# Kernel optimization log

Hardware: AMD Instinct MI355X
Metric: run time of the kernel (lower is better)

The kernel has to match this reference:

```python
import jax, jax.numpy as jnp
import numpy as np
import math

B, S, HID = 4, 2048, 1024
H, D = 16, HID // 16


def setup_inputs() -> dict:
    key = jax.random.key(0)
    ks = jax.random.split(key, 6)
    scale = 0.02
    inp = {
        "hidden_states": jax.random.normal(ks[0], (B, S, HID), dtype=jnp.float32),
        "Wq": jax.random.normal(ks[1], (HID, HID), dtype=jnp.float32) * scale,
        "bq": jnp.zeros((HID,), dtype=jnp.float32),
        "Wk1": jax.random.normal(ks[2], (HID, HID), dtype=jnp.float32) * scale,
        "bk1": jnp.zeros((HID,), dtype=jnp.float32),
        "Wk2": jax.random.normal(ks[3], (HID, HID), dtype=jnp.float32) * scale,
        "bk2": jnp.zeros((HID,), dtype=jnp.float32),
        "Wv1": jax.random.normal(ks[4], (HID, HID), dtype=jnp.float32) * scale,
        "bv1": jnp.zeros((HID,), dtype=jnp.float32),
        "Wv2": jax.random.normal(ks[5], (HID, HID), dtype=jnp.float32) * scale,
        "bv2": jnp.zeros((HID,), dtype=jnp.float32),
    }
    return inp


def _heads(x):
    # [B, S, HID] -> [B, H, S, D]
    return x.reshape(B, S, H, D).transpose(0, 2, 1, 3)


def reference(hidden_states, Wq, bq, Wk1, bk1, Wk2, bk2, Wv1, bv1, Wv2, bv2):
    # nn.Linear uses y = x @ W^T + b
    q = _heads(hidden_states @ Wq.T + bq)
    k1 = _heads(hidden_states @ Wk1.T + bk1)
    k2 = _heads(hidden_states @ Wk2.T + bk2)
    v1 = _heads(hidden_states @ Wv1.T + bv1)
    v2 = _heads(hidden_states @ Wv2.T + bv2)

    inv_sqrt_d = 1.0 / math.sqrt(D)
    scores = jnp.einsum('bhqd,bhkd->bhqk', q, k1) * inv_sqrt_d  # [B,H,S,S]
    probs = jax.nn.softmax(scores, axis=-1)
    ctx = jnp.einsum('bhqk,bhkd->bhqd', probs, v1)              # [B,H,S,D]
    ctx = jnp.einsum('bhqd,bhkd->bhqk', ctx, k2)                # [B,H,S,S]
    ctx = jnp.einsum('bhqk,bhkd->bhqd', ctx, v2)                # [B,H,S,D]
    # [B,H,S,D] -> [B,S,HID]
    return ctx.transpose(0, 2, 1, 3).reshape(B, S, HID)
```

## Files before the change

kernel.cpp:

```cpp
#include <hip/hip_runtime.h>
#include <hip/hip_bf16.h>

#define HIDD 1024
#define BATCH 4
#define SEQ 2048
#define NHEAD 16
#define HD 64
#define NW 5
#define MROWS (BATCH*SEQ)
#define NCOLS (NW*HIDD)

typedef __attribute__((ext_vector_type(8))) short bf16x8;
typedef __attribute__((ext_vector_type(4))) float f32x4;
typedef __attribute__((ext_vector_type(16))) float f32x16;
typedef __attribute__((ext_vector_type(4))) unsigned int uint4v;

__device__ __forceinline__ unsigned short f2b(float f) {
    __hip_bfloat16 h = __float2bfloat16(f);
    return __builtin_bit_cast(unsigned short, h);
}
__device__ __forceinline__ float b2f(unsigned short u) {
    __hip_bfloat16 h = __builtin_bit_cast(__hip_bfloat16, u);
    return __bfloat162float(h);
}

#if __has_builtin(__builtin_amdgcn_exp2f)
#define EXP2(x) __builtin_amdgcn_exp2f(x)
#else
#define EXP2(x) exp2f(x)
#endif

typedef __attribute__((address_space(1))) const void gvoid;
typedef __attribute__((address_space(3))) void lvoid;
__device__ __forceinline__ void gload16(const void* src, void* dst) {
    __builtin_amdgcn_global_load_lds((gvoid*)src, (lvoid*)dst, 16, 0, 0);
}

__global__ void cvt_kernel(const float* __restrict__ X,
                           const float* __restrict__ W0, const float* __restrict__ W1,
                           const float* __restrict__ W2, const float* __restrict__ W3,
                           const float* __restrict__ W4,
                           unsigned short* __restrict__ Xb, unsigned short* __restrict__ Wb)
{
    const int XN = MROWS * HIDD / 4;
    const int WN = HIDD * HIDD / 4;
    int i = blockIdx.x * 256 + threadIdx.x;
    if (i >= XN + 5 * WN) return;
    const float* src; unsigned short* dst; int off;
    if (i < XN) { src = X; dst = Xb; off = i; }
    else {
        int j = i - XN; int w = j / WN; int r = j - w * WN;
        src = (w == 0 ? W0 : w == 1 ? W1 : w == 2 ? W2 : w == 3 ? W3 : W4);
        dst = Wb + (long)w * HIDD * HIDD; off = r;
    }
    float4 v = ((const float4*)src)[off];
    short4 o;
    o.x = (short)f2b(v.x); o.y = (short)f2b(v.y);
    o.z = (short)f2b(v.z); o.w = (short)f2b(v.w);
    ((short4*)dst)[off] = o;
}

#define READ_A(buf, kh, mh) \
    _Pragma("unroll") \
    for (int mt = 0; mt < 4; ++mt) \
        af[mt] = *(const bf16x8*)((const char*)As[buf][kh] + \
                  (wr * 128 + (mh) * 64 + mt * 16 + q) * 64 + ((g ^ csw) << 4));
#define READ_B(buf, kh) \
    _Pragma("unroll") \
    for (int nt = 0; nt < 4; ++nt) \
        bfr[nt] = *(const bf16x8*)((const char*)Bs[buf][kh] + \
                  (wc * 64 + nt * 16 + q) * 64 + ((g ^ csw) << 4));
#define MFMA_Q(mh) \
    __builtin_amdgcn_s_setprio(1); \
    _Pragma("unroll") \
    for (int mt = 0; mt < 4; ++mt) \
    _Pragma("unroll") \
    for (int nt = 0; nt < 4; ++nt) \
        acc[(mh) * 4 + mt][nt] = __builtin_amdgcn_mfma_f32_16x16x32_bf16( \
            af[mt], bfr[nt], acc[(mh) * 4 + mt][nt], 0, 0, 0); \
    __builtin_amdgcn_s_setprio(0);

__global__ __launch_bounds__(512, 2) void gemm_proj(
    const unsigned short* __restrict__ Xb, const unsigned short* __restrict__ Wb,
    const float* __restrict__ pb0, const float* __restrict__ pb1, const float* __restrict__ pb2,
    const float* __restrict__ pb3, const float* __restrict__ pb4,
    unsigned short* __restrict__ C)
{
    __shared__ __align__(16) unsigned short As[2][2][256 * 32];
    __shared__ __align__(16) unsigned short Bs[2][2][256 * 32];
    int tid = threadIdx.x;
    int n = blockIdx.x;
    int xcd = n & 7, op = n >> 3;
    int ntile = (op < 16) ? 2 : 1;
    int lane = tid & 63, w = tid >> 6;
    int wr = w >> 2, wc = w & 3;
    int q = lane & 15, g = lane >> 4;
    int csw = (q >> 1) & 3;
    int srow = tid >> 2;
    int scol = ((tid & 3) ^ ((tid >> 3) & 3)) * 8;

    for (int tix = 0; tix < ntile; ++tix) {
        int o = op + tix * 64;
        int bm = xcd * 4 + (o & 3);
        int bn = o >> 2;

        if (tix) {
            asm volatile("s_waitcnt lgkmcnt(0)" ::: "memory");
            asm volatile("s_barrier" ::: "memory");
        }

        f32x4 acc[8][4] = {};
        const unsigned short* Ag = Xb + (long)(bm * 256) * HIDD;
        const unsigned short* Bg = Wb + (long)(bn * 256) * HIDD;

        auto stage = [&](const unsigned short* G, unsigned short* slot, int kc) {
#pragma unroll
            for (int l = 0; l < 2; ++l)
                gload16(G + (long)(l * 128 + srow) * HIDD + kc + scol,
                        (char*)slot + (l * 512 + tid) * 16);
        };

        stage(Ag, As[0][0], 0);
        stage(Bg, Bs[0][0], 0);
        stage(Ag, As[0][1], 32);
        stage(Bg, Bs[0][1], 32);
        stage(Ag, As[1][0], 64);
        stage(Bg, Bs[1][0], 64);

        for (int t = 0; t < 16; ++t) {
            int buf = t & 1;
            int kc1 = ((t + 1) & 15) * 64;
            int kc2 = ((t + 2) & 15) * 64;
            bf16x8 af[4], bfr[4];
            asm volatile("s_waitcnt vmcnt(8)" ::: "memory");
            asm volatile("s_waitcnt lgkmcnt(0)" ::: "memory");
            asm volatile("s_barrier" ::: "memory");
            READ_A(buf, 0, 0)
            READ_B(buf, 0)
            stage(Ag, As[buf ^ 1][1], kc1 + 32);
            MFMA_Q(0)
            READ_A(buf, 0, 1)
            stage(Bg, Bs[buf ^ 1][1], kc1 + 32);
            MFMA_Q(1)
            asm volatile("s_waitcnt vmcnt(8)" ::: "memory");
            asm volatile("s_waitcnt lgkmcnt(0)" ::: "memory");
            asm volatile("s_barrier" ::: "memory");
            READ_A(buf, 1, 0)
            READ_B(buf, 1)
            stage(Ag, As[buf][0], kc2);
            MFMA_Q(0)
            READ_A(buf, 1, 1)
            stage(Bg, Bs[buf][0], kc2);
            MFMA_Q(1)
        }

        int ncol0 = bn * 256 + wc * 64 + q;
        const float* bp = (bn < 4 ? pb0 : bn < 8 ? pb1 : bn < 12 ? pb2 : bn < 16 ? pb3 : pb4);
#pragma unroll
        for (int nt = 0; nt < 4; ++nt) {
            int ncol = ncol0 + nt * 16;
            float bv = bp[ncol & 1023];
#pragma unroll
            for (int mt = 0; mt < 8; ++mt) {
                int row = bm * 256 + wr * 128 + mt * 16 + g * 4;
#pragma unroll
                for (int r = 0; r < 4; ++r)
                    C[(long)(row + r) * NCOLS + ncol] = f2b(acc[mt][nt][r] + bv);
            }
        }
    }
}

#define QSCALE 0.180336880f
#define LDV 72
#define NT (SEQ / 64)

__global__ __launch_bounds__(512, 2) void flash1(
    const unsigned short* __restrict__ C, unsigned short* __restrict__ ctx)
{
    __shared__ unsigned short Ks[2][64 * 64];
    __shared__ unsigned short Vs[2][64 * LDV];
    __shared__ float Lbuf[8][32];
    int tid = threadIdx.x;
    int lane = tid & 63, w = tid >> 6;
    int q32 = lane & 31, hi = lane >> 5;
    int n = blockIdx.x;
    int qt = (n >> 3) & 7;
    int bh = (n & 7) * 8 + (n >> 6);
    int b = bh >> 4, h = bh & 15;
    long rowbase = (long)(b * SEQ) * NCOLS;
    int s0 = qt * 256;

    const unsigned short* Kg = C + rowbase + 1 * HIDD + h * 64;
    const unsigned short* Vg = C + rowbase + 3 * HIDD + h * 64;

    int krlo = lane >> 3;
    int kch  = (lane & 7) ^ krlo;
    int kp = tid & 31, dc = tid >> 5;
    int rsw = q32 & 7;

    bf16x8 qreg[4];
    {
        const unsigned short* Qp = C + rowbase + (long)(s0 + w * 32 + q32) * NCOLS + h * 64;
#pragma unroll
        for (int s = 0; s < 4; ++s) {
            bf16x8 v = *(const bf16x8*)(Qp + s * 16 + hi * 8);
#pragma unroll
            for (int j = 0; j < 8; j++)
                v[j] = (short)f2b(b2f((unsigned short)v[j]) * QSCALE);
            qreg[s] = v;
        }
    }

    gload16(Kg + (long)(w * 8 + krlo) * NCOLS + kch * 8,
            (char*)Ks[0] + w * 1024 + (lane << 4));
    if (tid < 256) {
        const unsigned short* vsrc = Vg + (long)(2 * kp) * NCOLS + dc * 8;
        bf16x8 v0 = *(const bf16x8*)vsrc;
        bf16x8 v1 = *(const bf16x8*)(vsrc + NCOLS);
        unsigned int* VsW = (unsigned int*)Vs[0];
#pragma unroll
        for (int j = 0; j < 8; j++) {
            unsigned int pk = ((unsigned int)(unsigned short)v0[j]) |
                              (((unsigned int)(unsigned short)v1[j]) << 16);
            VsW[(dc * 8 + j) * (LDV / 2) + kp] = pk;
        }
    }
    __syncthreads();

    f32x16 O0 = {}, O1 = {};
    float l_run = 0.f;

    auto body = [&](int kt, int cur, int nxt) {
        int ktn = (kt + 1) & (NT - 1);
        gload16(Kg + (long)(ktn * 64 + w * 8 + krlo) * NCOLS + kch * 8,
                (char*)Ks[nxt] + w * 1024 + (lane << 4));
        bf16x8 nv0 = {}, nv1 = {};
        if (tid < 256) {
            const unsigned short* nsrc = Vg + (long)(ktn * 64 + 2 * kp) * NCOLS + dc * 8;
            nv0 = *(const bf16x8*)nsrc;
            nv1 = *(const bf16x8*)(nsrc + NCOLS);
        }

        float lsum = 0.f;
        __builtin_amdgcn_s_setprio(1);
#pragma unroll
        for (int kb = 0; kb < 2; ++kb) {
            f32x16 st = {};
#pragma unroll
            for (int s = 0; s < 4; ++s) {
                bf16x8 kf = *(const bf16x8*)((const char*)Ks[cur] +
                             ((kb * 32 + q32) << 7) + (((2 * s + hi) ^ rsw) << 4));
                st = __builtin_amdgcn_mfma_f32_32x32x16_bf16(kf, qreg[s], st, 0, 0, 0);
            }
            float e[16];
#pragma unroll
            for (int r = 0; r < 16; ++r) e[r] = EXP2(st[r]);
            lsum += (((e[0]+e[1])+(e[2]+e[3])) + ((e[4]+e[5])+(e[6]+e[7])))
                  + (((e[8]+e[9])+(e[10]+e[11])) + ((e[12]+e[13])+(e[14]+e[15])));
            unsigned int Cw[8];
#pragma unroll
            for (int p = 0; p < 8; ++p)
                asm("v_cvt_pk_bf16_f32 %0, %1, %2" : "=v"(Cw[p]) : "v"(e[2*p]), "v"(e[2*p+1]));
#pragma unroll
            for (int t2 = 0; t2 < 2; ++t2) {
                unsigned int a0 = Cw[t2*4+0], a1 = Cw[t2*4+1];
                unsigned int a2 = Cw[t2*4+2], a3 = Cw[t2*4+3];
                asm("v_permlane32_swap_b32 %0, %1" : "+v"(a0), "+v"(a2));
                asm("v_permlane32_swap_b32 %0, %1" : "+v"(a1), "+v"(a3));
                uint4v aw; aw[0] = a0; aw[1] = a1; aw[2] = a2; aw[3] = a3;
                bf16x8 af = __builtin_bit_cast(bf16x8, aw);
                int t = kb * 2 + t2;
#pragma unroll
                for (int nt = 0; nt < 2; ++nt) {
                    bf16x8 vf = *(const bf16x8*)((const char*)Vs[cur] +
                                 (nt * 32 + q32) * (LDV * 2) + t * 32 + hi * 16);
                    if (nt == 0) O0 = __builtin_amdgcn_mfma_f32_32x32x16_bf16(af, vf, O0, 0, 0, 0);
                    else         O1 = __builtin_amdgcn_mfma_f32_32x32x16_bf16(af, vf, O1, 0, 0, 0);
                }
            }
        }
        __builtin_amdgcn_s_setprio(0);
        l_run += lsum;
        if (tid < 256) {
            unsigned int* VsWn = (unsigned int*)Vs[nxt];
#pragma unroll
            for (int j = 0; j < 8; ++j) {
                unsigned int pk = ((unsigned int)(unsigned short)nv0[j]) |
                                  (((unsigned int)(unsigned short)nv1[j]) << 16);
                VsWn[(dc * 8 + j) * (LDV / 2) + kp] = pk;
            }
        }
        __syncthreads();
    };

    for (int kt = 0; kt < NT; kt += 2) {
        body(kt, 0, 1);
        body(kt + 1, 1, 0);
    }

    l_run += __shfl_xor(l_run, 32);
    float linv = 1.f / l_run;
    Lbuf[w][q32] = linv;
    asm volatile("s_waitcnt lgkmcnt(0)" ::: "memory");
#pragma unroll
    for (int reg = 0; reg < 16; ++reg) {
        int row = (reg & 3) + 8 * (reg >> 2) + 4 * hi;
        float lr = Lbuf[w][row];
        unsigned short* dst = ctx + ((long)bh * SEQ + s0 + w * 32 + row) * 64 + q32;
        dst[0]  = f2b(O0[reg] * lr);
        dst[32] = f2b(O1[reg] * lr);
    }
}

#define LDT2 72
__global__ __launch_bounds__(256) void m_partial(
    const unsigned short* __restrict__ C, float* __restrict__ part)
{
    __shared__ unsigned short Kt[64 * LDT2];
    __shared__ unsigned short Vt[64 * LDT2];
    int tid = threadIdx.x;
    int lane = tid & 63, w = tid >> 6;
    int q32 = lane & 31, hi = lane >> 5;
    int sc = blockIdx.x;
    int bh = blockIdx.y; int b = bh >> 4, h = bh & 15;
    const unsigned short* K2 = C + (long)(b * SEQ) * NCOLS + 2 * HIDD + h * 64;
    const unsigned short* V2 = C + (long)(b * SEQ) * NCOLS + 4 * HIDD + h * 64;
    int kp = tid & 31, dc = tid >> 5;
    int d2h = w >> 1, d1h = w & 1;
    unsigned int* KtW = (unsigned int*)Kt;
    unsigned int* VtW = (unsigned int*)Vt;
    f32x16 acc = {};

    for (int tk = 0; tk < 4; ++tk) {
        int sbase = sc * 256 + tk * 64;
        if (tk) __syncthreads();
        const unsigned short* ks = K2 + (long)(sbase + 2 * kp) * NCOLS + dc * 8;
        bf16x8 k0 = *(const bf16x8*)ks, k1 = *(const bf16x8*)(ks + NCOLS);
        const unsigned short* vs = V2 + (long)(sbase + 2 * kp) * NCOLS + dc * 8;
        bf16x8 v0 = *(const bf16x8*)vs, v1 = *(const bf16x8*)(vs + NCOLS);
#pragma unroll
        for (int j = 0; j < 8; ++j) {
            KtW[(dc * 8 + j) * (LDT2 / 2) + kp] =
                (unsigned int)(unsigned short)k0[j] | ((unsigned int)(unsigned short)k1[j] << 16);
            VtW[(dc * 8 + j) * (LDT2 / 2) + kp] =
                (unsigned int)(unsigned short)v0[j] | ((unsigned int)(unsigned short)v1[j] << 16);
        }
        __syncthreads();
#pragma unroll
        for (int t = 0; t < 4; ++t) {
            bf16x8 afr = *(const bf16x8*)(Vt + (d2h * 32 + q32) * LDT2 + t * 16 + hi * 8);
            bf16x8 bfr = *(const bf16x8*)(Kt + (d1h * 32 + q32) * LDT2 + t * 16 + hi * 8);
            acc = __builtin_amdgcn_mfma_f32_32x32x16_bf16(afr, bfr, acc, 0, 0, 0);
        }
    }
    float* dst = part + ((long)(sc * 64 + bh) << 12);
#pragma unroll
    for (int reg = 0; reg < 16; ++reg) {
        int d2 = d2h * 32 + (reg & 3) + 8 * (reg >> 2) + 4 * hi;
        dst[d2 * 64 + d1h * 32 + q32] = acc[reg];
    }
}

__global__ void m_reduce(const float* __restrict__ part, float* __restrict__ MT)
{
    int i = blockIdx.x * 256 + threadIdx.x;
    if (i >= 64 * 4096) return;
    int bh = i >> 12, e = i & 4095;
    float s = 0.f;
#pragma unroll
    for (int sc = 0; sc < 8; sc++) s += part[((long)(sc * 64 + bh) << 12) + e];
    MT[i] = s;
}

#define LDF 72
#define LDM 68
__global__ __launch_bounds__(256) void final_out(
    const unsigned short* __restrict__ ctx, const float* __restrict__ MT,
    float* __restrict__ out)
{
    __shared__ unsigned short cs[64 * LDF];
    __shared__ float msT[64 * LDM];
    int tid = threadIdx.x;
    int st0 = blockIdx.x * 4;
    int bh = blockIdx.y; int b = bh >> 4, h = bh & 15;
    {
        const float* Msrc = MT + ((long)bh << 12);
        for (int i = tid; i < 4096; i += 256)
            msT[(i & 63) * LDM + (i >> 6)] = Msrc[i];
    }
    int s4 = (tid & 15) * 4, j4 = (tid >> 4) * 4;
    for (int ti = 0; ti < 4; ++ti) {
        int st = st0 + ti;
        if (ti) __syncthreads();
        {
            int i = tid >> 2, dcx = tid & 3;
            const unsigned short* src = ctx + ((long)bh * SEQ + st * 64 + i) * 64 + dcx * 16;
            *(int4*)(cs + i * LDF + dcx * 16)     = *(const int4*)src;
            *(int4*)(cs + i * LDF + dcx * 16 + 8) = *(const int4*)(src + 8);
        }
        __syncthreads();
        f32x4 acc[4] = {};
        for (int d1b = 0; d1b < 8; ++d1b) {
            bf16x8 cv[4];
#pragma unroll
            for (int r = 0; r < 4; ++r)
                cv[r] = *(const bf16x8*)(cs + (s4 + r) * LDF + d1b * 8);
#pragma unroll
            for (int dd = 0; dd < 8; ++dd) {
                f32x4 mj = *(const f32x4*)(msT + (d1b * 8 + dd) * LDM + j4);
#pragma unroll
                for (int r = 0; r < 4; ++r) {
                    float c = b2f((unsigned short)cv[r][dd]);
#pragma unroll
                    for (int j = 0; j < 4; ++j)
                        acc[r][j] += c * mj[j];
                }
            }
        }
        float* dst0 = out + (long)(b * SEQ + st * 64) * HIDD + h * 64;
#pragma unroll
        for (int r = 0; r < 4; ++r)
            *(f32x4*)(dst0 + (long)(s4 + r) * HIDD + j4) = acc[r];
    }
}

extern "C" void kernel_launch(void* const* d_in, const int* in_sizes, int n_in,
                              void* d_out, int out_size, void* d_ws, size_t ws_size,
                              hipStream_t stream)
{
    const float* X   = (const float*)d_in[0];
    const float* Wq  = (const float*)d_in[1];
    const float* bq  = (const float*)d_in[2];
    const float* Wk1 = (const float*)d_in[3];
    const float* bk1 = (const float*)d_in[4];
    const float* Wk2 = (const float*)d_in[5];
    const float* bk2 = (const float*)d_in[6];
    const float* Wv1 = (const float*)d_in[7];
    const float* bv1 = (const float*)d_in[8];
    const float* Wv2 = (const float*)d_in[9];
    const float* bv2 = (const float*)d_in[10];

    char* ws = (char*)d_ws;
    unsigned short* Xb  = (unsigned short*)(ws);
    unsigned short* Wb  = (unsigned short*)(ws + 16777216);
    unsigned short* C   = (unsigned short*)(ws + 27262976);
    unsigned short* ctx = (unsigned short*)(ws + 111149056);
    float* part         = (float*)(ws + 127926272);
    float* MT           = (float*)(ws + 136314880);
    float* out = (float*)d_out;

    cvt_kernel<<<dim3(13312), 256, 0, stream>>>(X, Wq, Wk1, Wk2, Wv1, Wv2, Xb, Wb);
    gemm_proj<<<dim3(512), 512, 0, stream>>>(Xb, Wb, bq, bk1, bk2, bv1, bv2, C);
    flash1<<<dim3(512), 512, 0, stream>>>(C, ctx);
    m_partial<<<dim3(8, 64), 256, 0, stream>>>(C, part);
    m_reduce<<<dim3(1024), 256, 0, stream>>>(part, MT);
    final_out<<<dim3(8, 64), 256, 0, stream>>>(ctx, MT, out);
}
```

Baseline: 243.6 us.

## Load projection GEMM B operand directly from global memory into registers

The weight (B) tile in the projection GEMM no longer goes through shared memory. Each wave now reads its B fragments straight from global memory into registers just before its MFMAs, and only the activation (A) tile is still staged in LDS, with the vmcnt waits adjusted to match. This removes the B staging traffic and halves the kernel's LDS use. In exchange, global-load latency is exposed directly in front of the MFMAs. Waves that share a column slice also fetch the same B data redundantly from cache instead of sharing one LDS copy.

```diff
diff --git a/kernel.cpp b/kernel.cpp
--- a/kernel.cpp
+++ b/kernel.cpp
@@ -65,11 +65,10 @@
     for (int mt = 0; mt < 4; ++mt) \
         af[mt] = *(const bf16x8*)((const char*)As[buf][kh] + \
                   (wr * 128 + (mh) * 64 + mt * 16 + q) * 64 + ((g ^ csw) << 4));
-#define READ_B(buf, kh) \
+#define READ_B_G(t, kh) \
     _Pragma("unroll") \
     for (int nt = 0; nt < 4; ++nt) \
-        bfr[nt] = *(const bf16x8*)((const char*)Bs[buf][kh] + \
-                  (wc * 64 + nt * 16 + q) * 64 + ((g ^ csw) << 4));
+        bfr[nt] = *(const bf16x8*)(Bw + (long)(nt * 16) * HIDD + (t) * 64 + (kh) * 32 + g * 8);
 #define MFMA_Q(mh) \
     __builtin_amdgcn_s_setprio(1); \
     _Pragma("unroll") \
@@ -87,7 +86,6 @@
     unsigned short* __restrict__ C)
 {
     __shared__ __align__(16) unsigned short As[2][2][256 * 32];
-    __shared__ __align__(16) unsigned short Bs[2][2][256 * 32];
     int tid = threadIdx.x;
     int n = blockIdx.x;
     int xcd = n & 7, op = n >> 3;
@@ -111,46 +109,41 @@
 
         f32x4 acc[8][4] = {};
         const unsigned short* Ag = Xb + (long)(bm * 256) * HIDD;
-        const unsigned short* Bg = Wb + (long)(bn * 256) * HIDD;
-
-        auto stage = [&](const unsigned short* G, unsigned short* slot, int kc) {
+        const unsigned short* Bw = Wb + (long)(bn * 256 + wc * 64 + q) * HIDD;
+
+        auto stage = [&](unsigned short* slot, int kc) {
 #pragma unroll
             for (int l = 0; l < 2; ++l)
-                gload16(G + (long)(l * 128 + srow) * HIDD + kc + scol,
+                gload16(Ag + (long)(l * 128 + srow) * HIDD + kc + scol,
                         (char*)slot + (l * 512 + tid) * 16);
         };
 
-        stage(Ag, As[0][0], 0);
-        stage(Bg, Bs[0][0], 0);
-        stage(Ag, As[0][1], 32);
-        stage(Bg, Bs[0][1], 32);
-        stage(Ag, As[1][0], 64);
-        stage(Bg, Bs[1][0], 64);
+        stage(As[0][0], 0);
+        stage(As[0][1], 32);
+        stage(As[1][0], 64);
 
         for (int t = 0; t < 16; ++t) {
             int buf = t & 1;
             int kc1 = ((t + 1) & 15) * 64;
             int kc2 = ((t + 2) & 15) * 64;
             bf16x8 af[4], bfr[4];
-            asm volatile("s_waitcnt vmcnt(8)" ::: "memory");
+            asm volatile("s_waitcnt vmcnt(2)" ::: "memory");
             asm volatile("s_waitcnt lgkmcnt(0)" ::: "memory");
             asm volatile("s_barrier" ::: "memory");
+            READ_B_G(t, 0)
             READ_A(buf, 0, 0)
-            READ_B(buf, 0)
-            stage(Ag, As[buf ^ 1][1], kc1 + 32);
+            stage(As[buf ^ 1][1], kc1 + 32);
             MFMA_Q(0)
             READ_A(buf, 0, 1)
-            stage(Bg, Bs[buf ^ 1][1], kc1 + 32);
             MFMA_Q(1)
-            asm volatile("s_waitcnt vmcnt(8)" ::: "memory");
+            asm volatile("s_waitcnt vmcnt(2)" ::: "memory");
             asm volatile("s_waitcnt lgkmcnt(0)" ::: "memory");
             asm volatile("s_barrier" ::: "memory");
+            READ_B_G(t, 1)
             READ_A(buf, 1, 0)
-            READ_B(buf, 1)
-            stage(Ag, As[buf][0], kc2);
+            stage(As[buf][0], kc2);
             MFMA_Q(0)
             READ_A(buf, 1, 1)
-            stage(Bg, Bs[buf][0], kc2);
             MFMA_Q(1)
         }
 
```

After: 293.6 us. 20.5% more time.

## Merge flash and K2V2 partial kernels into one launch, fold reduce into final

Applied to the files above, without the earlier changes.

Merges the flash attention kernel and the K2^T V2 partial-product kernel into a single launch of 1024 blocks, where the first 512 blocks run attention and the rest compute partials. The separate reduction kernel is removed, and final_out now sums the 8 partials itself while loading M. This cuts two kernel launches and lets the small partial work fill idle CUs during the flash tail. In exchange, the partial blocks run at 512 threads with half of them idle and share the flash kernel's larger LDS footprint, and every final_out block redundantly re-reduces its head's partials.

```diff
diff --git a/kernel.cpp b/kernel.cpp
--- a/kernel.cpp
+++ b/kernel.cpp
@@ -174,209 +174,203 @@
 #define QSCALE 0.180336880f
 #define LDV 72
 #define NT (SEQ / 64)
-
-__global__ __launch_bounds__(512, 2) void flash1(
-    const unsigned short* __restrict__ C, unsigned short* __restrict__ ctx)
+#define LDT2 72
+
+__global__ __launch_bounds__(512, 2) void flash_mp(
+    const unsigned short* __restrict__ C, unsigned short* __restrict__ ctx,
+    float* __restrict__ part)
 {
     __shared__ unsigned short Ks[2][64 * 64];
     __shared__ unsigned short Vs[2][64 * LDV];
     __shared__ float Lbuf[8][32];
-    int tid = threadIdx.x;
-    int lane = tid & 63, w = tid >> 6;
-    int q32 = lane & 31, hi = lane >> 5;
-    int n = blockIdx.x;
-    int qt = (n >> 3) & 7;
-    int bh = (n & 7) * 8 + (n >> 6);
-    int b = bh >> 4, h = bh & 15;
-    long rowbase = (long)(b * SEQ) * NCOLS;
-    int s0 = qt * 256;
-
-    const unsigned short* Kg = C + rowbase + 1 * HIDD + h * 64;
-    const unsigned short* Vg = C + rowbase + 3 * HIDD + h * 64;
-
-    int krlo = lane >> 3;
-    int kch  = (lane & 7) ^ krlo;
-    int kp = tid & 31, dc = tid >> 5;
-    int rsw = q32 & 7;
-
-    bf16x8 qreg[4];
-    {
-        const unsigned short* Qp = C + rowbase + (long)(s0 + w * 32 + q32) * NCOLS + h * 64;
-#pragma unroll
-        for (int s = 0; s < 4; ++s) {
-            bf16x8 v = *(const bf16x8*)(Qp + s * 16 + hi * 8);
-#pragma unroll
-            for (int j = 0; j < 8; j++)
-                v[j] = (short)f2b(b2f((unsigned short)v[j]) * QSCALE);
-            qreg[s] = v;
-        }
-    }
-
-    gload16(Kg + (long)(w * 8 + krlo) * NCOLS + kch * 8,
-            (char*)Ks[0] + w * 1024 + (lane << 4));
-    if (tid < 256) {
-        const unsigned short* vsrc = Vg + (long)(2 * kp) * NCOLS + dc * 8;
-        bf16x8 v0 = *(const bf16x8*)vsrc;
-        bf16x8 v1 = *(const bf16x8*)(vsrc + NCOLS);
-        unsigned int* VsW = (unsigned int*)Vs[0];
-#pragma unroll
-        for (int j = 0; j < 8; j++) {
-            unsigned int pk = ((unsigned int)(unsigned short)v0[j]) |
-                              (((unsigned int)(unsigned short)v1[j]) << 16);
-            VsW[(dc * 8 + j) * (LDV / 2) + kp] = pk;
-        }
-    }
-    __syncthreads();
-
-    f32x16 O0 = {}, O1 = {};
-    float l_run = 0.f;
-
-    auto body = [&](int kt, int cur, int nxt) {
-        int ktn = (kt + 1) & (NT - 1);
-        gload16(Kg + (long)(ktn * 64 + w * 8 + krlo) * NCOLS + kch * 8,
-                (char*)Ks[nxt] + w * 1024 + (lane << 4));
-        bf16x8 nv0 = {}, nv1 = {};
-        if (tid < 256) {
-            const unsigned short* nsrc = Vg + (long)(ktn * 64 + 2 * kp) * NCOLS + dc * 8;
-            nv0 = *(const bf16x8*)nsrc;
-            nv1 = *(const bf16x8*)(nsrc + NCOLS);
-        }
-
-        float lsum = 0.f;
-        __builtin_amdgcn_s_setprio(1);
-#pragma unroll
-        for (int kb = 0; kb < 2; ++kb) {
-            f32x16 st = {};
-#pragma unroll
-            for (int s = 0; s < 4; ++s) {
-                bf16x8 kf = *(const bf16x8*)((const char*)Ks[cur] +
-                             ((kb * 32 + q32) << 7) + (((2 * s + hi) ^ rsw) << 4));
-                st = __builtin_amdgcn_mfma_f32_32x32x16_bf16(kf, qreg[s], st, 0, 0, 0);
-            }
-            float e[16];
-#pragma unroll
-            for (int r = 0; r < 16; ++r) e[r] = EXP2(st[r]);
-            lsum += (((e[0]+e[1])+(e[2]+e[3])) + ((e[4]+e[5])+(e[6]+e[7])))
-                  + (((e[8]+e[9])+(e[10]+e[11])) + ((e[12]+e[13])+(e[14]+e[15])));
-            unsigned int Cw[8];
-#pragma unroll
-            for (int p = 0; p < 8; ++p)
-                asm("v_cvt_pk_bf16_f32 %0, %1, %2" : "=v"(Cw[p]) : "v"(e[2*p]), "v"(e[2*p+1]));
-#pragma unroll
-            for (int t2 = 0; t2 < 2; ++t2) {
-                unsigned int a0 = Cw[t2*4+0], a1 = Cw[t2*4+1];
-                unsigned int a2 = Cw[t2*4+2], a3 = Cw[t2*4+3];
-                asm("v_permlane32_swap_b32 %0, %1" : "+v"(a0), "+v"(a2));
-                asm("v_permlane32_swap_b32 %0, %1" : "+v"(a1), "+v"(a3));
-                uint4v aw; aw[0] = a0; aw[1] = a1; aw[2] = a2; aw[3] = a3;
-                bf16x8 af = __builtin_bit_cast(bf16x8, aw);
-                int t = kb * 2 + t2;
-#pragma unroll
-                for (int nt = 0; nt < 2; ++nt) {
-                    bf16x8 vf = *(const bf16x8*)((const char*)Vs[cur] +
-                                 (nt * 32 + q32) * (LDV * 2) + t * 32 + hi * 16);
-                    if (nt == 0) O0 = __builtin_amdgcn_mfma_f32_32x32x16_bf16(af, vf, O0, 0, 0, 0);
-                    else         O1 = __builtin_amdgcn_mfma_f32_32x32x16_bf16(af, vf, O1, 0, 0, 0);
-                }
-            }
-        }
-        __builtin_amdgcn_s_setprio(0);
-        l_run += lsum;
-        if (tid < 256) {
-            unsigned int* VsWn = (unsigned int*)Vs[nxt];
-#pragma unroll
-            for (int j = 0; j < 8; ++j) {
-                unsigned int pk = ((unsigned int)(unsigned short)nv0[j]) |
-                                  (((unsigned int)(unsigned short)nv1[j]) << 16);
-                VsWn[(dc * 8 + j) * (LDV / 2) + kp] = pk;
-            }
-        }
-        __syncthreads();
-    };
-
-    for (int kt = 0; kt < NT; kt += 2) {
-        body(kt, 0, 1);
-        body(kt + 1, 1, 0);
-    }
-
-    l_run += __shfl_xor(l_run, 32);
-    float linv = 1.f / l_run;
-    Lbuf[w][q32] = linv;
-    asm volatile("s_waitcnt lgkmcnt(0)" ::: "memory");
-#pragma unroll
-    for (int reg = 0; reg < 16; ++reg) {
-        int row = (reg & 3) + 8 * (reg >> 2) + 4 * hi;
-        float lr = Lbuf[w][row];
-        unsigned short* dst = ctx + ((long)bh * SEQ + s0 + w * 32 + row) * 64 + q32;
-        dst[0]  = f2b(O0[reg] * lr);
-        dst[32] = f2b(O1[reg] * lr);
-    }
-}
-
-#define LDT2 72
-__global__ __launch_bounds__(256) void m_partial(
-    const unsigned short* __restrict__ C, float* __restrict__ part)
-{
     __shared__ unsigned short Kt[64 * LDT2];
     __shared__ unsigned short Vt[64 * LDT2];
     int tid = threadIdx.x;
     int lane = tid & 63, w = tid >> 6;
     int q32 = lane & 31, hi = lane >> 5;
-    int sc = blockIdx.x;
-    int bh = blockIdx.y; int b = bh >> 4, h = bh & 15;
-    const unsigned short* K2 = C + (long)(b * SEQ) * NCOLS + 2 * HIDD + h * 64;
-    const unsigned short* V2 = C + (long)(b * SEQ) * NCOLS + 4 * HIDD + h * 64;
-    int kp = tid & 31, dc = tid >> 5;
-    int d2h = w >> 1, d1h = w & 1;
-    unsigned int* KtW = (unsigned int*)Kt;
-    unsigned int* VtW = (unsigned int*)Vt;
-    f32x16 acc = {};
-
-    for (int tk = 0; tk < 4; ++tk) {
-        int sbase = sc * 256 + tk * 64;
-        if (tk) __syncthreads();
-        const unsigned short* ks = K2 + (long)(sbase + 2 * kp) * NCOLS + dc * 8;
-        bf16x8 k0 = *(const bf16x8*)ks, k1 = *(const bf16x8*)(ks + NCOLS);
-        const unsigned short* vs = V2 + (long)(sbase + 2 * kp) * NCOLS + dc * 8;
-        bf16x8 v0 = *(const bf16x8*)vs, v1 = *(const bf16x8*)(vs + NCOLS);
-#pragma unroll
-        for (int j = 0; j < 8; ++j) {
-            KtW[(dc * 8 + j) * (LDT2 / 2) + kp] =
-                (unsigned int)(unsigned short)k0[j] | ((unsigned int)(unsigned short)k1[j] << 16);
-            VtW[(dc * 8 + j) * (LDT2 / 2) + kp] =
-                (unsigned int)(unsigned short)v0[j] | ((unsigned int)(unsigned short)v1[j] << 16);
+
+    if (blockIdx.x < 512) {
+        int n = blockIdx.x;
+        int qt = (n >> 3) & 7;
+        int bh = (n & 7) * 8 + (n >> 6);
+        int b = bh >> 4, h = bh & 15;
+        long rowbase = (long)(b * SEQ) * NCOLS;
+        int s0 = qt * 256;
+
+        const unsigned short* Kg = C + rowbase + 1 * HIDD + h * 64;
+        const unsigned short* Vg = C + rowbase + 3 * HIDD + h * 64;
+
+        int krlo = lane >> 3;
+        int kch  = (lane & 7) ^ krlo;
+        int kp = tid & 31, dc = tid >> 5;
+        int rsw = q32 & 7;
+
+        bf16x8 qreg[4];
+        {
+            const unsigned short* Qp = C + rowbase + (long)(s0 + w * 32 + q32) * NCOLS + h * 64;
+#pragma unroll
+            for (int s = 0; s < 4; ++s) {
+                bf16x8 v = *(const bf16x8*)(Qp + s * 16 + hi * 8);
+#pragma unroll
+                for (int j = 0; j < 8; j++)
+                    v[j] = (short)f2b(b2f((unsigned short)v[j]) * QSCALE);
+                qreg[s] = v;
+            }
+        }
+
+        gload16(Kg + (long)(w * 8 + krlo) * NCOLS + kch * 8,
+                (char*)Ks[0] + w * 1024 + (lane << 4));
+        if (tid < 256) {
+            const unsigned short* vsrc = Vg + (long)(2 * kp) * NCOLS + dc * 8;
+            bf16x8 v0 = *(const bf16x8*)vsrc;
+            bf16x8 v1 = *(const bf16x8*)(vsrc + NCOLS);
+            unsigned int* VsW = (unsigned int*)Vs[0];
+#pragma unroll
+            for (int j = 0; j < 8; j++) {
+                unsigned int pk = ((unsigned int)(unsigned short)v0[j]) |
+                                  (((unsigned int)(unsigned short)v1[j]) << 16);
+                VsW[(dc * 8 + j) * (LDV / 2) + kp] = pk;
+            }
         }
         __syncthreads();
-#pragma unroll
-        for (int t = 0; t < 4; ++t) {
-            bf16x8 afr = *(const bf16x8*)(Vt + (d2h * 32 + q32) * LDT2 + t * 16 + hi * 8);
-            bf16x8 bfr = *(const bf16x8*)(Kt + (d1h * 32 + q32) * LDT2 + t * 16 + hi * 8);
-            acc = __builtin_amdgcn_mfma_f32_32x32x16_bf16(afr, bfr, acc, 0, 0, 0);
+
+        f32x16 O0 = {}, O1 = {};
+        float l_run = 0.f;
+
+        auto body = [&](int kt, int cur, int nxt) {
+            int ktn = (kt + 1) & (NT - 1);
+            gload16(Kg + (long)(ktn * 64 + w * 8 + krlo) * NCOLS + kch * 8,
+                    (char*)Ks[nxt] + w * 1024 + (lane << 4));
+            bf16x8 nv0 = {}, nv1 = {};
+            if (tid < 256) {
+                const unsigned short* nsrc = Vg + (long)(ktn * 64 + 2 * kp) * NCOLS + dc * 8;
+                nv0 = *(const bf16x8*)nsrc;
+                nv1 = *(const bf16x8*)(nsrc + NCOLS);
+            }
+
+            float lsum = 0.f;
+            __builtin_amdgcn_s_setprio(1);
+#pragma unroll
+            for (int kb = 0; kb < 2; ++kb) {
+                f32x16 st = {};
+#pragma unroll
+                for (int s = 0; s < 4; ++s) {
+                    bf16x8 kf = *(const bf16x8*)((const char*)Ks[cur] +
+                                 ((kb * 32 + q32) << 7) + (((2 * s + hi) ^ rsw) << 4));
+                    st = __builtin_amdgcn_mfma_f32_32x32x16_bf16(kf, qreg[s], st, 0, 0, 0);
+                }
+                float e[16];
+#pragma unroll
+                for (int r = 0; r < 16; ++r) e[r] = EXP2(st[r]);
+                lsum += (((e[0]+e[1])+(e[2]+e[3])) + ((e[4]+e[5])+(e[6]+e[7])))
+                      + (((e[8]+e[9])+(e[10]+e[11])) + ((e[12]+e[13])+(e[14]+e[15])));
+                unsigned int Cw[8];
+#pragma unroll
+                for (int p = 0; p < 8; ++p)
+                    asm("v_cvt_pk_bf16_f32 %0, %1, %2" : "=v"(Cw[p]) : "v"(e[2*p]), "v"(e[2*p+1]));
+#pragma unroll
+                for (int t2 = 0; t2 < 2; ++t2) {
+                    unsigned int a0 = Cw[t2*4+0], a1 = Cw[t2*4+1];
+                    unsigned int a2 = Cw[t2*4+2], a3 = Cw[t2*4+3];
+                    asm("v_permlane32_swap_b32 %0, %1" : "+v"(a0), "+v"(a2));
+                    asm("v_permlane32_swap_b32 %0, %1" : "+v"(a1), "+v"(a3));
+                    uint4v aw; aw[0] = a0; aw[1] = a1; aw[2] = a2; aw[3] = a3;
+                    bf16x8 af = __builtin_bit_cast(bf16x8, aw);
+                    int t = kb * 2 + t2;
+#pragma unroll
+                    for (int nt = 0; nt < 2; ++nt) {
+                        bf16x8 vf = *(const bf16x8*)((const char*)Vs[cur] +
+                                     (nt * 32 + q32) * (LDV * 2) + t * 32 + hi * 16);
+                        if (nt == 0) O0 = __builtin_amdgcn_mfma_f32_32x32x16_bf16(af, vf, O0, 0, 0, 0);
+                        else         O1 = __builtin_amdgcn_mfma_f32_32x32x16_bf16(af, vf, O1, 0, 0, 0);
+                    }
+                }
+            }
+            __builtin_amdgcn_s_setprio(0);
+            l_run += lsum;
+            if (tid < 256) {
+                unsigned int* VsWn = (unsigned int*)Vs[nxt];
+#pragma unroll
+                for (int j = 0; j < 8; ++j) {
+                    unsigned int pk = ((unsigned int)(unsigned short)nv0[j]) |
+                                      (((unsigned int)(unsigned short)nv1[j]) << 16);
+                    VsWn[(dc * 8 + j) * (LDV / 2) + kp] = pk;
+                }
+            }
+            __syncthreads();
+        };
+
+        for (int kt = 0; kt < NT; kt += 2) {
+            body(kt, 0, 1);
+            body(kt + 1, 1, 0);
+        }
+
+        l_run += __shfl_xor(l_run, 32);
+        float linv = 1.f / l_run;
+        Lbuf[w][q32] = linv;
+        asm volatile("s_waitcnt lgkmcnt(0)" ::: "memory");
+#pragma unroll
+        for (int reg = 0; reg < 16; ++reg) {
+            int row = (reg & 3) + 8 * (reg >> 2) + 4 * hi;
+            float lr = Lbuf[w][row];
+            unsigned short* dst = ctx + ((long)bh * SEQ + s0 + w * 32 + row) * 64 + q32;
+            dst[0]  = f2b(O0[reg] * lr);
+            dst[32] = f2b(O1[reg] * lr);
+        }
+    } else {
+        int idx = blockIdx.x - 512;
+        int sc = idx & 7;
+        int bh = idx >> 3;
+        int b = bh >> 4, h = bh & 15;
+        const unsigned short* K2 = C + (long)(b * SEQ) * NCOLS + 2 * HIDD + h * 64;
+        const unsigned short* V2 = C + (long)(b * SEQ) * NCOLS + 4 * HIDD + h * 64;
+        int kp = tid & 31, dc = tid >> 5;
+        int d2h = w >> 1, d1h = w & 1;
+        unsigned int* KtW = (unsigned int*)Kt;
+        unsigned int* VtW = (unsigned int*)Vt;
+        f32x16 acc = {};
+
+        for (int tk = 0; tk < 4; ++tk) {
+            int sbase = sc * 256 + tk * 64;
+            if (tk) __syncthreads();
+            if (tid < 256) {
+                const unsigned short* ks = K2 + (long)(sbase + 2 * kp) * NCOLS + dc * 8;
+                bf16x8 k0 = *(const bf16x8*)ks, k1 = *(const bf16x8*)(ks + NCOLS);
+                const unsigned short* vs = V2 + (long)(sbase + 2 * kp) * NCOLS + dc * 8;
+                bf16x8 v0 = *(const bf16x8*)vs, v1 = *(const bf16x8*)(vs + NCOLS);
+#pragma unroll
+                for (int j = 0; j < 8; ++j) {
+                    KtW[(dc * 8 + j) * (LDT2 / 2) + kp] =
+                        (unsigned int)(unsigned short)k0[j] | ((unsigned int)(unsigned short)k1[j] << 16);
+                    VtW[(dc * 8 + j) * (LDT2 / 2) + kp] =
+                        (unsigned int)(unsigned short)v0[j] | ((unsigned int)(unsigned short)v1[j] << 16);
+                }
+            }
+            __syncthreads();
+            if (tid < 256) {
+#pragma unroll
+                for (int t = 0; t < 4; ++t) {
+                    bf16x8 afr = *(const bf16x8*)(Vt + (d2h * 32 + q32) * LDT2 + t * 16 + hi * 8);
+                    bf16x8 bfr = *(const bf16x8*)(Kt + (d1h * 32 + q32) * LDT2 + t * 16 + hi * 8);
+                    acc = __builtin_amdgcn_mfma_f32_32x32x16_bf16(afr, bfr, acc, 0, 0, 0);
+                }
+            }
+        }
+        if (tid < 256) {
+            float* dst = part + ((long)(sc * 64 + bh) << 12);
+#pragma unroll
+            for (int reg = 0; reg < 16; ++reg) {
+                int d2 = d2h * 32 + (reg & 3) + 8 * (reg >> 2) + 4 * hi;
+                dst[d2 * 64 + d1h * 32 + q32] = acc[reg];
+            }
         }
     }
-    float* dst = part + ((long)(sc * 64 + bh) << 12);
-#pragma unroll
-    for (int reg = 0; reg < 16; ++reg) {
-        int d2 = d2h * 32 + (reg & 3) + 8 * (reg >> 2) + 4 * hi;
-        dst[d2 * 64 + d1h * 32 + q32] = acc[reg];
-    }
-}
-
-__global__ void m_reduce(const float* __restrict__ part, float* __restrict__ MT)
-{
-    int i = blockIdx.x * 256 + threadIdx.x;
-    if (i >= 64 * 4096) return;
-    int bh = i >> 12, e = i & 4095;
-    float s = 0.f;
-#pragma unroll
-    for (int sc = 0; sc < 8; sc++) s += part[((long)(sc * 64 + bh) << 12) + e];
-    MT[i] = s;
 }
 
 #define LDF 72
 #define LDM 68
 __global__ __launch_bounds__(256) void final_out(
-    const unsigned short* __restrict__ ctx, const float* __restrict__ MT,
+    const unsigned short* __restrict__ ctx, const float* __restrict__ part,
     float* __restrict__ out)
 {
     __shared__ unsigned short cs[64 * LDF];
@@ -385,9 +379,13 @@
     int st0 = blockIdx.x * 4;
     int bh = blockIdx.y; int b = bh >> 4, h = bh & 15;
     {
-        const float* Msrc = MT + ((long)bh << 12);
-        for (int i = tid; i < 4096; i += 256)
-            msT[(i & 63) * LDM + (i >> 6)] = Msrc[i];
+        for (int i = tid; i < 4096; i += 256) {
+            float s = 0.f;
+#pragma unroll
+            for (int sc = 0; sc < 8; sc++)
+                s += part[((long)(sc * 64 + bh) << 12) + i];
+            msT[(i & 63) * LDM + (i >> 6)] = s;
+        }
     }
     int s4 = (tid & 15) * 4, j4 = (tid >> 4) * 4;
     for (int ti = 0; ti < 4; ++ti) {
@@ -447,13 +445,10 @@
     unsigned short* C   = (unsigned short*)(ws + 27262976);
     unsigned short* ctx = (unsigned short*)(ws + 111149056);
     float* part         = (float*)(ws + 127926272);
-    float* MT           = (float*)(ws + 136314880);
     float* out = (float*)d_out;
 
     cvt_kernel<<<dim3(13312), 256, 0, stream>>>(X, Wq, Wk1, Wk2, Wv1, Wv2, Xb, Wb);
     gemm_proj<<<dim3(512), 512, 0, stream>>>(Xb, Wb, bq, bk1, bk2, bv1, bv2, C);
-    flash1<<<dim3(512), 512, 0, stream>>>(C, ctx);
-    m_partial<<<dim3(8, 64), 256, 0, stream>>>(C, part);
-    m_reduce<<<dim3(1024), 256, 0, stream>>>(part, MT);
-    final_out<<<dim3(8, 64), 256, 0, stream>>>(ctx, MT, out);
-}
+    flash_mp<<<dim3(1024), 512, 0, stream>>>(C, ctx, part);
+    final_out<<<dim3(8, 64), 256, 0, stream>>>(ctx, part, out);
+}
```

Result: no change. 246.7 us (+1.3%).
